# Performance work log

Hardware: AMD Instinct MI355X
Metric: run time of the kernel (lower is better)

The kernel has to match this reference:

```python
import jax, jax.numpy as jnp
import numpy as np

B, S, DIM, H, D = 2, 2048, 1024, 16, 64
WINDOW = 512
MAX_MEM_SEGMENTS = 1
ROPE_THETA = 10000.0


def _rope(t, pos):
    # lucidrains rotary-embedding-torch default: interleaved pairs
    d = t.shape[-1]
    inv_freq = 1.0 / (ROPE_THETA ** (jnp.arange(0, d, 2, dtype=jnp.float32) / d))
    freqs = pos[:, None].astype(jnp.float32) * inv_freq[None, :]        # [S, d/2]
    freqs = jnp.repeat(freqs, 2, axis=-1)                               # [S, d]
    cos, sin = jnp.cos(freqs), jnp.sin(freqs)
    t1, t2 = t[..., 0::2], t[..., 1::2]
    rot = jnp.stack((-t2, t1), axis=-1).reshape(t.shape)                # rotate_half
    return t * cos + rot * sin


def setup_inputs() -> dict:
    key = jax.random.key(0)
    ks = jax.random.split(key, 8)
    tokens = jax.random.normal(ks[0], (B, S, DIM), dtype=jnp.float32)
    value_residual = jax.random.normal(ks[1], (B, H, S, D), dtype=jnp.float32)
    episode_ids = jnp.sort(jax.random.randint(ks[2], (B, S), 0, 4), axis=-1)
    w = 0.02
    Wq = jax.random.normal(ks[3], (DIM, H * D), dtype=jnp.float32) * w
    Wkv = jax.random.normal(ks[4], (DIM, 2 * H * D), dtype=jnp.float32) * w
    Wo = jax.random.normal(ks[5], (H * D, DIM), dtype=jnp.float32) * w
    Wg = jax.random.normal(ks[6], (DIM, H), dtype=jnp.float32) * w
    Wmix = jax.random.normal(ks[7], (DIM, H), dtype=jnp.float32) * w
    return {"tokens": tokens, "value_residual": value_residual, "episode_ids": episode_ids,
            "Wq": Wq, "Wkv": Wkv, "Wo": Wo, "Wg": Wg, "Wmix": Wmix}


def reference(tokens, value_residual, episode_ids, Wq, Wkv, Wo, Wg, Wmix):
    b, s, _ = tokens.shape
    scale = D ** -0.5

    def split_heads(x):  # [b, n, h*d] -> [b, h, n, d]
        return x.reshape(b, s, H, D).transpose(0, 2, 1, 3)

    q = split_heads(tokens @ Wq)
    kv = tokens @ Wkv
    k, v = split_heads(kv[..., :H * D]), split_heads(kv[..., H * D:])

    q = q * scale

    # value-residual lerp: v.lerp(value_residual, mix)
    mix = jax.nn.sigmoid(jnp.einsum('bnd,dh->bhn', tokens, Wmix))[..., None]  # [b,h,n,1]
    v = v + mix * (value_residual - v)

    pos = jnp.arange(s)
    q = _rope(q, pos)
    k = _rope(k, pos)

    sim = jnp.einsum('bhid,bhjd->bhij', q, k)

    # fixed-window causal mask: masked where dist < 0 or dist > max_mem_segments*window
    dist = pos[:, None] - pos[None, :]
    win_mask = (dist < 0) | (dist > MAX_MEM_SEGMENTS * WINDOW)            # [s, s]
    ep_mask = episode_ids[:, :, None] != episode_ids[:, None, :]          # [b, s, s]
    mask = win_mask[None, None, :, :] | ep_mask[:, None, :, :]

    sim = jnp.where(mask, -jnp.finfo(sim.dtype).max, sim)
    attn = jax.nn.softmax(sim, axis=-1)
    out = jnp.einsum('bhij,bhjd->bhid', attn, v)

    # sigmoid value gating
    gate = jax.nn.sigmoid(jnp.einsum('bnd,dh->bhn', tokens, Wg))[..., None]
    out = out * gate

    out = out.transpose(0, 2, 1, 3).reshape(b, s, H * D)
    return out @ Wo
```

## Files before the change

kernel.cpp:

```cpp
#include <hip/hip_runtime.h>
#include <math.h>

#define BB 2
#define SS 2048
#define DIMM 1024
#define HH 16
#define DD 64
#define WINDOW 512

typedef __bf16 bf16x8 __attribute__((ext_vector_type(8)));
typedef __bf16 bf16x4 __attribute__((ext_vector_type(4)));
typedef float f32x4 __attribute__((ext_vector_type(4)));

__device__ __forceinline__ unsigned short f2bf(float f) {
    unsigned int u = __float_as_uint(f);
    u = (u + 0x7FFFu + ((u >> 16) & 1u)) >> 16;
    return (unsigned short)u;
}
__device__ __forceinline__ float bf2f(unsigned short u) {
    return __uint_as_float((unsigned int)u << 16);
}

__device__ __forceinline__ void async_cp16(unsigned short* lds_dst, const unsigned short* g_src) {
    __builtin_amdgcn_global_load_lds(
        (const __attribute__((address_space(1))) unsigned int*)g_src,
        (__attribute__((address_space(3))) unsigned int*)lds_dst, 16, 0, 0);
}

__global__ __launch_bounds__(256) void prep_all_kernel(
    const float* __restrict__ tokens, unsigned short* __restrict__ tokA,
    const float* __restrict__ Wq, const float* __restrict__ Wkv,
    const float* __restrict__ Wo, unsigned short* __restrict__ BtW,
    unsigned short* __restrict__ WotW,
    const float* __restrict__ Wg, const float* __restrict__ Wmix,
    unsigned short* __restrict__ wgmt,
    const int* __restrict__ ep, int* __restrict__ epstart,
    float2* __restrict__ ropetab)
{
    int bid = blockIdx.x;
    int tid = threadIdx.x;
    if (bid < 4096) {
        const float* src;
        unsigned short* dst;
        int C, bx, by;
        if (bid < 1024) {
            src = Wq; dst = BtW; C = 1024; bx = bid & 31; by = bid >> 5;
        } else if (bid < 3072) {
            int rel = bid - 1024;
            src = Wkv; dst = BtW + 1024 * 1024; C = 2048; bx = rel & 63; by = rel >> 6;
        } else {
            int rel = bid - 3072;
            src = Wo; dst = WotW; C = 1024; bx = rel & 31; by = rel >> 5;
        }
        const int R = 1024;
        __shared__ float t[32][33];
        int c0 = bx * 32, r0 = by * 32;
        int tx = tid & 31, ty = tid >> 5;
        #pragma unroll
        for (int u = 0; u < 4; ++u)
            t[ty + 8 * u][tx] = src[(size_t)(r0 + ty + 8 * u) * C + c0 + tx];
        __syncthreads();
        #pragma unroll
        for (int u = 0; u < 4; ++u)
            dst[(size_t)(c0 + ty + 8 * u) * R + r0 + tx] = f2bf(t[tx][ty + 8 * u]);
    } else if (bid < 6144) {
        const int n4 = (BB * SS * DIMM) / 4;
        for (int i = (bid - 4096) * 256 + tid; i < n4; i += 2048 * 256) {
            float4 v = ((const float4*)tokens)[i];
            ushort4 o;
            o.x = f2bf(v.x); o.y = f2bf(v.y); o.z = f2bf(v.z); o.w = f2bf(v.w);
            ((ushort4*)tokA)[i] = o;
        }
    } else if (bid < 6272) {
        int idx = (bid - 6144) * 256 + tid;
        int n = idx >> 10, k = idx & 1023;
        const float* src = (n < 16) ? Wg : Wmix;
        wgmt[idx] = f2bf(src[k * HH + (n & 15)]);
    } else if (bid < 6288) {
        int idx = (bid - 6272) * 256 + tid;
        int b = idx >> 11, i = idx & 2047;
        const int* e = ep + b * SS;
        int v = e[i];
        int lo = 0, hi = i;
        while (lo < hi) {
            int mid = (lo + hi) >> 1;
            if (e[mid] == v) hi = mid; else lo = mid + 1;
        }
        epstart[idx] = lo;
    } else {
        int idx = (bid - 6288) * 256 + tid;
        int s = idx >> 5, p = idx & 31;
        float invf = powf(10000.f, -(float)(2 * p) * (1.f / 64.f));
        float ang = (float)s * invf;
        float rr = ang - 6.2831853f * floorf(ang * 0.15915494f);
        float cs, sn;
        __sincosf(rr, &sn, &cs);
        ropetab[idx] = make_float2(cs, sn);
    }
}

__global__ __launch_bounds__(256) void projmix_kernel(
    const unsigned short* __restrict__ A, const unsigned short* __restrict__ Bt,
    unsigned short* __restrict__ qo, unsigned short* __restrict__ ko,
    unsigned short* __restrict__ vo,
    const unsigned short* __restrict__ wgmt,
    float* __restrict__ gate, float* __restrict__ mix)
{
    __shared__ unsigned short As[2][128 * 32];
    __shared__ unsigned short Bs[2][128 * 32];
    __shared__ float red[4][16][32];

    const int K = 1024;
    int bid = blockIdx.x;
    int tid = threadIdx.x;
    int lane = tid & 63;
    int wave = tid >> 6;
    int fr = lane & 15, hi = lane >> 4;

    if (bid < 768) {
        int nbase = (bid % 24) * 128;
        int mbase = (bid / 24) * 128;
        int wr = wave >> 1, wc = wave & 1;

        int srow = tid >> 2;
        int sp   = tid & 3;
        int scol = (sp ^ ((srow >> 1) & 3)) * 8;
        const unsigned short* agp0 = A  + (size_t)(mbase + srow) * K + scol;
        const unsigned short* agp1 = A  + (size_t)(mbase + srow + 64) * K + scol;
        const unsigned short* bgp0 = Bt + (size_t)(nbase + srow) * K + scol;
        const unsigned short* bgp1 = Bt + (size_t)(nbase + srow + 64) * K + scol;

        f32x4 acc[4][4];
        #pragma unroll
        for (int m_ = 0; m_ < 4; ++m_)
            #pragma unroll
            for (int n_ = 0; n_ < 4; ++n_)
                acc[m_][n_] = (f32x4){0.f, 0.f, 0.f, 0.f};

        int aidx[4], bidx[4];
        #pragma unroll
        for (int m_ = 0; m_ < 4; ++m_) {
            int row = wr * 64 + m_ * 16 + fr;
            aidx[m_] = row * 32 + (hi ^ ((row >> 1) & 3)) * 8;
        }
        #pragma unroll
        for (int n_ = 0; n_ < 4; ++n_) {
            int row = wc * 64 + n_ * 16 + fr;
            bidx[n_] = row * 32 + (hi ^ ((row >> 1) & 3)) * 8;
        }

        auto stage = [&](int buf, int k0) {
            async_cp16(&As[buf][tid * 8], agp0 + k0);
            async_cp16(&As[buf][2048 + tid * 8], agp1 + k0);
            async_cp16(&Bs[buf][tid * 8], bgp0 + k0);
            async_cp16(&Bs[buf][2048 + tid * 8], bgp1 + k0);
        };

        stage(0, 0);
        for (int k0 = 0; k0 < K; k0 += 32) {
            int cur = (k0 >> 5) & 1;
            __syncthreads();
            if (k0 + 32 < K) stage(cur ^ 1, k0 + 32);

            bf16x8 af[4], bfr[4];
            #pragma unroll
            for (int m_ = 0; m_ < 4; ++m_) af[m_] = *(const bf16x8*)&As[cur][aidx[m_]];
            #pragma unroll
            for (int n_ = 0; n_ < 4; ++n_) bfr[n_] = *(const bf16x8*)&Bs[cur][bidx[n_]];
            #pragma unroll
            for (int m_ = 0; m_ < 4; ++m_)
                #pragma unroll
                for (int n_ = 0; n_ < 4; ++n_)
                    acc[m_][n_] = __builtin_amdgcn_mfma_f32_16x16x32_bf16(
                        af[m_], bfr[n_], acc[m_][n_], 0, 0, 0);
        }

        #pragma unroll
        for (int m_ = 0; m_ < 4; ++m_) {
            #pragma unroll
            for (int n_ = 0; n_ < 4; ++n_) {
                int c = nbase + wc * 64 + n_ * 16 + fr;
                int cc = c & 1023, h = cc >> 6, d = cc & 63;
                unsigned short* dst = (c < 1024) ? qo : (c < 2048) ? ko : vo;
                #pragma unroll
                for (int j = 0; j < 4; ++j) {
                    int mg = mbase + wr * 64 + m_ * 16 + hi * 4 + j;
                    int b = mg >> 11, s = mg & 2047;
                    dst[(((size_t)b * HH + h) * SS + s) * DD + d] = f2bf(acc[m_][n_][j]);
                }
            }
        }
    } else {
        int mbase = (bid - 768) * 16;
        int kw = wave * 256;

        f32x4 acc[2];
        acc[0] = (f32x4){0.f, 0.f, 0.f, 0.f};
        acc[1] = (f32x4){0.f, 0.f, 0.f, 0.f};

        const unsigned short* a0 = A + (size_t)(mbase + fr) * 1024 + kw + hi * 8;
        const unsigned short* b0 = wgmt + (size_t)fr * 1024 + kw + hi * 8;
        const unsigned short* b1 = wgmt + (size_t)(16 + fr) * 1024 + kw + hi * 8;

        #pragma unroll 2
        for (int k = 0; k < 256; k += 32) {
            bf16x8 af0 = *(const bf16x8*)(a0 + k);
            bf16x8 bf0 = *(const bf16x8*)(b0 + k);
            bf16x8 bf1 = *(const bf16x8*)(b1 + k);
            acc[0] = __builtin_amdgcn_mfma_f32_16x16x32_bf16(af0, bf0, acc[0], 0, 0, 0);
            acc[1] = __builtin_amdgcn_mfma_f32_16x16x32_bf16(af0, bf1, acc[1], 0, 0, 0);
        }

        #pragma unroll
        for (int n_ = 0; n_ < 2; ++n_)
            #pragma unroll
            for (int j = 0; j < 4; ++j)
                red[wave][hi * 4 + j][n_ * 16 + fr] = acc[n_][j];
        __syncthreads();

        #pragma unroll
        for (int e = 0; e < 2; ++e) {
            int idx = tid * 2 + e;
            int r = idx >> 5, c = idx & 31;
            float s4 = red[0][r][c] + red[1][r][c] + red[2][r][c] + red[3][r][c];
            float sg = 1.f / (1.f + __expf(-s4));
            int mg = mbase + r;
            int b = mg >> 11, s = mg & 2047;
            int h = c & 15;
            float* dst = (c < 16) ? gate : mix;
            dst[((size_t)b * HH + h) * SS + s] = sg;
        }
    }
}

template<int BM, int BN>
__global__ __launch_bounds__(256) void gemm_mfma(
    const unsigned short* __restrict__ A, const unsigned short* __restrict__ Bt,
    float* __restrict__ C)
{
    const int K = 1024;
    constexpr int MFR = BM / 32;
    constexpr int NFR = BN / 32;
    int nbase = blockIdx.x * BN;
    int mbase = blockIdx.y * BM;

    int tid = threadIdx.x;
    int lane = tid & 63;
    int wave = tid >> 6;
    int wr = wave >> 1, wc = wave & 1;
    int fr = lane & 15, hi = lane >> 4;

    __shared__ unsigned short As[2][BM * 32];
    __shared__ unsigned short Bs[2][BN * 32];

    int srow = tid >> 2;
    int sp   = tid & 3;
    int scol = (sp ^ ((srow >> 1) & 3)) * 8;
    const unsigned short* agp0 = A  + (size_t)(mbase + srow) * K + scol;
    const unsigned short* agp1 = (BM == 128)
        ? A + (size_t)(mbase + srow + 64) * K + scol : agp0;
    const unsigned short* bgp0 = Bt + (size_t)(nbase + srow) * K + scol;
    const unsigned short* bgp1 = (BN == 128)
        ? Bt + (size_t)(nbase + srow + 64) * K + scol : bgp0;

    f32x4 acc[MFR][NFR];
    #pragma unroll
    for (int m_ = 0; m_ < MFR; ++m_)
        #pragma unroll
        for (int n_ = 0; n_ < NFR; ++n_)
            acc[m_][n_] = (f32x4){0.f, 0.f, 0.f, 0.f};

    int aidx[MFR], bidx[NFR];
    #pragma unroll
    for (int m_ = 0; m_ < MFR; ++m_) {
        int row = wr * (BM / 2) + m_ * 16 + fr;
        aidx[m_] = row * 32 + (hi ^ ((row >> 1) & 3)) * 8;
    }
    #pragma unroll
    for (int n_ = 0; n_ < NFR; ++n_) {
        int row = wc * (BN / 2) + n_ * 16 + fr;
        bidx[n_] = row * 32 + (hi ^ ((row >> 1) & 3)) * 8;
    }

    auto stage = [&](int buf, int k0) {
        async_cp16(&As[buf][tid * 8], agp0 + k0);
        if constexpr (BM == 128)
            async_cp16(&As[buf][2048 + tid * 8], agp1 + k0);
        async_cp16(&Bs[buf][tid * 8], bgp0 + k0);
        if constexpr (BN == 128)
            async_cp16(&Bs[buf][2048 + tid * 8], bgp1 + k0);
    };

    stage(0, 0);
    for (int k0 = 0; k0 < K; k0 += 32) {
        int cur = (k0 >> 5) & 1;
        __syncthreads();
        if (k0 + 32 < K) stage(cur ^ 1, k0 + 32);

        bf16x8 af[MFR], bfr[NFR];
        #pragma unroll
        for (int m_ = 0; m_ < MFR; ++m_) af[m_] = *(const bf16x8*)&As[cur][aidx[m_]];
        #pragma unroll
        for (int n_ = 0; n_ < NFR; ++n_) bfr[n_] = *(const bf16x8*)&Bs[cur][bidx[n_]];
        #pragma unroll
        for (int m_ = 0; m_ < MFR; ++m_)
            #pragma unroll
            for (int n_ = 0; n_ < NFR; ++n_)
                acc[m_][n_] = __builtin_amdgcn_mfma_f32_16x16x32_bf16(
                    af[m_], bfr[n_], acc[m_][n_], 0, 0, 0);
    }

    #pragma unroll
    for (int m_ = 0; m_ < MFR; ++m_) {
        #pragma unroll
        for (int n_ = 0; n_ < NFR; ++n_) {
            int c = nbase + wc * (BN / 2) + n_ * 16 + fr;
            #pragma unroll
            for (int j = 0; j < 4; ++j) {
                int mg = mbase + wr * (BM / 2) + m_ * 16 + hi * 4 + j;
                C[(size_t)mg * 1024 + c] = acc[m_][n_][j];
            }
        }
    }
}

__global__ __launch_bounds__(256) void rope_lerp_kernel(
    unsigned short* __restrict__ q, unsigned short* __restrict__ k,
    const unsigned short* __restrict__ v0, const float* __restrict__ vres,
    const float* __restrict__ mix, unsigned short* __restrict__ vt,
    const float2* __restrict__ ropetab)
{
    int st = blockIdx.x;
    int bh = blockIdx.y;
    int tid = threadIdx.x;
    int sl = tid >> 2;
    int dg = (tid & 3) * 16;
    int s = st * 64 + sl;
    size_t rowoff = ((size_t)bh * SS + s) * DD + dg;

    __shared__ unsigned short vtile[64][66];

    union { uint4 v[2]; unsigned short u[16]; } qa, ka, va;
    qa.v[0] = *(const uint4*)(q + rowoff);
    qa.v[1] = *(const uint4*)(q + rowoff + 8);
    ka.v[0] = *(const uint4*)(k + rowoff);
    ka.v[1] = *(const uint4*)(k + rowoff + 8);
    va.v[0] = *(const uint4*)(v0 + rowoff);
    va.v[1] = *(const uint4*)(v0 + rowoff + 8);
    float4 w[4];
    #pragma unroll
    for (int u = 0; u < 4; ++u) w[u] = *(const float4*)(vres + rowoff + 4 * u);
    float mx = mix[(size_t)bh * SS + s];
    const float2* tb = ropetab + (size_t)s * 32 + (dg >> 1);

    #pragma unroll
    for (int u = 0; u < 8; ++u) {
        float2 cssn = tb[u];
        float cs = cssn.x, sn = cssn.y;
        float x = bf2f(qa.u[2 * u]), y = bf2f(qa.u[2 * u + 1]);
        qa.u[2 * u]     = f2bf((x * cs - y * sn) * 0.125f);
        qa.u[2 * u + 1] = f2bf((y * cs + x * sn) * 0.125f);
        x = bf2f(ka.u[2 * u]); y = bf2f(ka.u[2 * u + 1]);
        ka.u[2 * u]     = f2bf(x * cs - y * sn);
        ka.u[2 * u + 1] = f2bf(y * cs + x * sn);
    }
    *(uint4*)(q + rowoff)     = qa.v[0];
    *(uint4*)(q + rowoff + 8) = qa.v[1];
    *(uint4*)(k + rowoff)     = ka.v[0];
    *(uint4*)(k + rowoff + 8) = ka.v[1];

    #pragma unroll
    for (int e = 0; e < 16; ++e) {
        float vv = bf2f(va.u[e]);
        float wr = ((const float*)w)[e];
        vtile[sl][dg + e] = f2bf(vv + mx * (wr - vv));
    }
    __syncthreads();

    int d = tid >> 2;
    int sseg = (tid & 3) * 16;
    union { uint4 v[2]; unsigned short u[16]; } ot;
    #pragma unroll
    for (int e = 0; e < 16; ++e) ot.u[e] = vtile[sseg + e][d];
    unsigned short* dst = vt + ((size_t)bh * DD + d) * SS + st * 64 + sseg;
    *(uint4*)dst = ot.v[0];
    *(uint4*)(dst + 8) = ot.v[1];
}

__global__ __launch_bounds__(512) void attn_mfma(
    const unsigned short* __restrict__ qbh, const unsigned short* __restrict__ kbh,
    const unsigned short* __restrict__ vt, const int* __restrict__ epstart,
    const float* __restrict__ gate, unsigned short* __restrict__ ao)
{
    int orig = blockIdx.x;
    int swz  = (orig & 7) * 64 + (orig >> 3);
    int bh = swz >> 4, qt = swz & 15;
    int b = bh >> 4, h = bh & 15;
    int q0 = qt * 128;
    int tid = threadIdx.x;
    int wave = tid >> 6, lane = tid & 63;
    int lq = lane & 15, lg = lane >> 4;
    int i = q0 + wave * 16 + lq;

    __shared__ unsigned short Ks[4096];
    __shared__ unsigned short Vs[4096];
    alignas(16) __shared__ unsigned short P_lds[8][16][72];

    int srow = tid >> 3;
    int sc = (((tid & 7) ^ (srow & 7)) << 3);
    const unsigned short* kS = kbh + ((size_t)bh * SS + srow) * DD + sc;
    const unsigned short* vS = vt + ((size_t)bh * DD + srow) * SS + sc;

    int fidx[4];
    #pragma unroll
    for (int n = 0; n < 4; ++n) {
        int r = 16 * n + lq;
        fidx[n] = r * 64 + ((lg ^ (r & 7)) << 3);
    }

    const unsigned short* qrow = qbh + ((size_t)bh * SS + i) * DD + lg * 8;
    bf16x8 bq0 = *(const bf16x8*)qrow;
    bf16x8 bq1 = *(const bf16x8*)(qrow + 32);

    int jmin = i - WINDOW;
    int es = epstart[b * SS + i];
    if (es > jmin) jmin = es;
    float gi = gate[(size_t)bh * SS + i];

    float m = -1e30f, l = 0.f;
    f32x4 o[4];
    #pragma unroll
    for (int n = 0; n < 4; ++n) o[n] = (f32x4){0.f, 0.f, 0.f, 0.f};

    int jt0 = (q0 >= 512) ? ((q0 - 512) >> 6) : 0;
    int jt1 = (q0 + 127) >> 6;
    int nt = jt1 - jt0 + 1;
    int jb0 = jt0 * 64;

    for (int u = 0; u < nt; ++u) {
        int jbase = jb0 + 64 * u;

        __syncthreads();
        async_cp16(&Ks[tid * 8], kS + (size_t)jbase * DD);
        async_cp16(&Vs[tid * 8], vS + jbase);
        __syncthreads();

        f32x4 acc[4];
        #pragma unroll
        for (int n = 0; n < 4; ++n) acc[n] = (f32x4){0.f, 0.f, 0.f, 0.f};
        __builtin_amdgcn_s_setprio(1);
        #pragma unroll
        for (int n = 0; n < 4; ++n) {
            bf16x8 kf0 = *(const bf16x8*)&Ks[fidx[n]];
            bf16x8 kf1 = *(const bf16x8*)&Ks[fidx[n] ^ 32];
            acc[n] = __builtin_amdgcn_mfma_f32_16x16x32_bf16(kf0, bq0, acc[n], 0, 0, 0);
            acc[n] = __builtin_amdgcn_mfma_f32_16x16x32_bf16(kf1, bq1, acc[n], 0, 0, 0);
        }
        __builtin_amdgcn_s_setprio(0);

        int jb = jbase + lg * 4;
        #pragma unroll
        for (int n = 0; n < 4; ++n)
            #pragma unroll
            for (int r = 0; r < 4; ++r) {
                int j = jb + 16 * n + r;
                if (j < jmin || j > i) acc[n][r] = -3e38f;
            }

        float tm = -3e38f;
        #pragma unroll
        for (int n = 0; n < 4; ++n)
            tm = fmaxf(tm, fmaxf(fmaxf(acc[n][0], acc[n][1]), fmaxf(acc[n][2], acc[n][3])));
        tm = fmaxf(tm, __shfl_xor(tm, 16, 64));
        tm = fmaxf(tm, __shfl_xor(tm, 32, 64));
        float mnew = fmaxf(m, tm);
        float scale = __expf(m - mnew);
        float ts = 0.f;
        #pragma unroll
        for (int n = 0; n < 4; ++n)
            #pragma unroll
            for (int r = 0; r < 4; ++r) {
                float p = __expf(acc[n][r] - mnew);
                acc[n][r] = p;
                ts += p;
            }
        ts += __shfl_xor(ts, 16, 64);
        ts += __shfl_xor(ts, 32, 64);
        l = l * scale + ts;
        m = mnew;
        #pragma unroll
        for (int n = 0; n < 4; ++n) o[n] = o[n] * scale;

        #pragma unroll
        for (int n = 0; n < 4; ++n) {
            bf16x4 pv;
            pv[0] = (__bf16)acc[n][0]; pv[1] = (__bf16)acc[n][1];
            pv[2] = (__bf16)acc[n][2]; pv[3] = (__bf16)acc[n][3];
            *(bf16x4*)&P_lds[wave][lq][16 * n + lg * 4] = pv;
        }
        bf16x8 bp0 = *(const bf16x8*)&P_lds[wave][lq][lg * 8];
        bf16x8 bp1 = *(const bf16x8*)&P_lds[wave][lq][32 + lg * 8];

        __builtin_amdgcn_s_setprio(1);
        #pragma unroll
        for (int n = 0; n < 4; ++n) {
            bf16x8 vf0 = *(const bf16x8*)&Vs[fidx[n]];
            bf16x8 vf1 = *(const bf16x8*)&Vs[fidx[n] ^ 32];
            o[n] = __builtin_amdgcn_mfma_f32_16x16x32_bf16(vf0, bp0, o[n], 0, 0, 0);
            o[n] = __builtin_amdgcn_mfma_f32_16x16x32_bf16(vf1, bp1, o[n], 0, 0, 0);
        }
        __builtin_amdgcn_s_setprio(0);
    }

    float g = gi / l;
    #pragma unroll
    for (int n = 0; n < 4; ++n) {
        bf16x4 ov;
        ov[0] = (__bf16)(o[n][0] * g); ov[1] = (__bf16)(o[n][1] * g);
        ov[2] = (__bf16)(o[n][2] * g); ov[3] = (__bf16)(o[n][3] * g);
        *(bf16x4*)(ao + (((size_t)b * SS + i) * HH + h) * DD + 16 * n + lg * 4) = ov;
    }
}

extern "C" void kernel_launch(void* const* d_in, const int* in_sizes, int n_in,
                              void* d_out, int out_size, void* d_ws, size_t ws_size,
                              hipStream_t stream)
{
    const float* tokens = (const float*)d_in[0];
    const float* vres   = (const float*)d_in[1];
    const int*   ep     = (const int*)d_in[2];
    const float* Wq     = (const float*)d_in[3];
    const float* Wkv    = (const float*)d_in[4];
    const float* Wo     = (const float*)d_in[5];
    const float* Wg     = (const float*)d_in[6];
    const float* Wmix   = (const float*)d_in[7];
    float* out = (float*)d_out;

    char* wsb = (char*)d_ws;
    unsigned short* qbh  = (unsigned short*)(wsb + 0);
    unsigned short* kbh  = (unsigned short*)(wsb + 8388608);
    unsigned short* vb0  = (unsigned short*)(wsb + 16777216);
    unsigned short* vtb  = (unsigned short*)(wsb + 25165824);
    unsigned short* aob  = (unsigned short*)(wsb + 33554432);
    unsigned short* tokA = (unsigned short*)(wsb + 41943040);
    unsigned short* BtW  = (unsigned short*)(wsb + 50331648);
    float* gatep = (float*)(wsb + 56623104);
    float* mixp  = (float*)(wsb + 56885248);
    int*   epst  = (int*)(wsb + 57147392);
    unsigned short* wgmt = (unsigned short*)(wsb + 57163776);
    unsigned short* WotW = (unsigned short*)(wsb + 57229312);
    float2* ropetab = (float2*)(wsb + 59326464);

    prep_all_kernel<<<6544, 256, 0, stream>>>(tokens, tokA, Wq, Wkv, Wo, BtW, WotW,
                                              Wg, Wmix, wgmt, ep, epst, ropetab);
    projmix_kernel<<<1024, 256, 0, stream>>>(tokA, BtW, qbh, kbh, vb0,
                                             wgmt, gatep, mixp);
    rope_lerp_kernel<<<dim3(SS / 64, BB * HH), 256, 0, stream>>>(qbh, kbh, vb0, vres, mixp, vtb, ropetab);
    attn_mfma<<<512, 512, 0, stream>>>(qbh, kbh, vtb, epst, gatep, aob);

    gemm_mfma<128, 64><<<dim3(16, 32), 256, 0, stream>>>(aob, WotW, out);
}
```

Baseline: 110.8 us.

## Fuse Q rotary embedding into attention kernel and alias projmix shared memory

```diff
diff --git a/kernel.cpp b/kernel.cpp
--- a/kernel.cpp
+++ b/kernel.cpp
@@ -106,9 +106,10 @@
     const unsigned short* __restrict__ wgmt,
     float* __restrict__ gate, float* __restrict__ mix)
 {
-    __shared__ unsigned short As[2][128 * 32];
-    __shared__ unsigned short Bs[2][128 * 32];
-    __shared__ float red[4][16][32];
+    __shared__ char smem[32768];
+    unsigned short* As = (unsigned short*)smem;
+    unsigned short* Bs = (unsigned short*)(smem + 16384);
+    float (*red)[16][32] = (float (*)[16][32])smem;
 
     const int K = 1024;
     int bid = blockIdx.x;
@@ -150,10 +151,10 @@
         }
 
         auto stage = [&](int buf, int k0) {
-            async_cp16(&As[buf][tid * 8], agp0 + k0);
-            async_cp16(&As[buf][2048 + tid * 8], agp1 + k0);
-            async_cp16(&Bs[buf][tid * 8], bgp0 + k0);
-            async_cp16(&Bs[buf][2048 + tid * 8], bgp1 + k0);
+            async_cp16(&As[buf * 4096 + tid * 8], agp0 + k0);
+            async_cp16(&As[buf * 4096 + 2048 + tid * 8], agp1 + k0);
+            async_cp16(&Bs[buf * 4096 + tid * 8], bgp0 + k0);
+            async_cp16(&Bs[buf * 4096 + 2048 + tid * 8], bgp1 + k0);
         };
 
         stage(0, 0);
@@ -164,9 +165,9 @@
 
             bf16x8 af[4], bfr[4];
             #pragma unroll
-            for (int m_ = 0; m_ < 4; ++m_) af[m_] = *(const bf16x8*)&As[cur][aidx[m_]];
-            #pragma unroll
-            for (int n_ = 0; n_ < 4; ++n_) bfr[n_] = *(const bf16x8*)&Bs[cur][bidx[n_]];
+            for (int m_ = 0; m_ < 4; ++m_) af[m_] = *(const bf16x8*)&As[cur * 4096 + aidx[m_]];
+            #pragma unroll
+            for (int n_ = 0; n_ < 4; ++n_) bfr[n_] = *(const bf16x8*)&Bs[cur * 4096 + bidx[n_]];
             #pragma unroll
             for (int m_ = 0; m_ < 4; ++m_)
                 #pragma unroll
@@ -325,7 +326,7 @@
 }
 
 __global__ __launch_bounds__(256) void rope_lerp_kernel(
-    unsigned short* __restrict__ q, unsigned short* __restrict__ k,
+    unsigned short* __restrict__ k,
     const unsigned short* __restrict__ v0, const float* __restrict__ vres,
     const float* __restrict__ mix, unsigned short* __restrict__ vt,
     const float2* __restrict__ ropetab)
@@ -340,9 +341,7 @@
 
     __shared__ unsigned short vtile[64][66];
 
-    union { uint4 v[2]; unsigned short u[16]; } qa, ka, va;
-    qa.v[0] = *(const uint4*)(q + rowoff);
-    qa.v[1] = *(const uint4*)(q + rowoff + 8);
+    union { uint4 v[2]; unsigned short u[16]; } ka, va;
     ka.v[0] = *(const uint4*)(k + rowoff);
     ka.v[1] = *(const uint4*)(k + rowoff + 8);
     va.v[0] = *(const uint4*)(v0 + rowoff);
@@ -357,15 +356,10 @@
     for (int u = 0; u < 8; ++u) {
         float2 cssn = tb[u];
         float cs = cssn.x, sn = cssn.y;
-        float x = bf2f(qa.u[2 * u]), y = bf2f(qa.u[2 * u + 1]);
-        qa.u[2 * u]     = f2bf((x * cs - y * sn) * 0.125f);
-        qa.u[2 * u + 1] = f2bf((y * cs + x * sn) * 0.125f);
-        x = bf2f(ka.u[2 * u]); y = bf2f(ka.u[2 * u + 1]);
+        float x = bf2f(ka.u[2 * u]), y = bf2f(ka.u[2 * u + 1]);
         ka.u[2 * u]     = f2bf(x * cs - y * sn);
         ka.u[2 * u + 1] = f2bf(y * cs + x * sn);
     }
-    *(uint4*)(q + rowoff)     = qa.v[0];
-    *(uint4*)(q + rowoff + 8) = qa.v[1];
     *(uint4*)(k + rowoff)     = ka.v[0];
     *(uint4*)(k + rowoff + 8) = ka.v[1];
 
@@ -390,7 +384,8 @@
 __global__ __launch_bounds__(512) void attn_mfma(
     const unsigned short* __restrict__ qbh, const unsigned short* __restrict__ kbh,
     const unsigned short* __restrict__ vt, const int* __restrict__ epstart,
-    const float* __restrict__ gate, unsigned short* __restrict__ ao)
+    const float* __restrict__ gate, unsigned short* __restrict__ ao,
+    const float2* __restrict__ ropetab)
 {
     int orig = blockIdx.x;
     int swz  = (orig & 7) * 64 + (orig >> 3);
@@ -419,8 +414,25 @@
     }
 
     const unsigned short* qrow = qbh + ((size_t)bh * SS + i) * DD + lg * 8;
-    bf16x8 bq0 = *(const bf16x8*)qrow;
-    bf16x8 bq1 = *(const bf16x8*)(qrow + 32);
+    union { bf16x8 v; __bf16 e[8]; } uq0, uq1;
+    uq0.v = *(const bf16x8*)qrow;
+    uq1.v = *(const bf16x8*)(qrow + 32);
+    {
+        const float2* tbq = ropetab + (size_t)i * 32 + lg * 4;
+        #pragma unroll
+        for (int p = 0; p < 4; ++p) {
+            float2 t0 = tbq[p];
+            float x = (float)uq0.e[2 * p], y = (float)uq0.e[2 * p + 1];
+            uq0.e[2 * p]     = (__bf16)((x * t0.x - y * t0.y) * 0.125f);
+            uq0.e[2 * p + 1] = (__bf16)((y * t0.x + x * t0.y) * 0.125f);
+            float2 t1 = tbq[16 + p];
+            x = (float)uq1.e[2 * p]; y = (float)uq1.e[2 * p + 1];
+            uq1.e[2 * p]     = (__bf16)((x * t1.x - y * t1.y) * 0.125f);
+            uq1.e[2 * p + 1] = (__bf16)((y * t1.x + x * t1.y) * 0.125f);
+        }
+    }
+    bf16x8 bq0 = uq0.v;
+    bf16x8 bq1 = uq1.v;
 
     int jmin = i - WINDOW;
     int es = epstart[b * SS + i];
@@ -555,8 +567,8 @@
                                               Wg, Wmix, wgmt, ep, epst, ropetab);
     projmix_kernel<<<1024, 256, 0, stream>>>(tokA, BtW, qbh, kbh, vb0,
                                              wgmt, gatep, mixp);
-    rope_lerp_kernel<<<dim3(SS / 64, BB * HH), 256, 0, stream>>>(qbh, kbh, vb0, vres, mixp, vtb, ropetab);
-    attn_mfma<<<512, 512, 0, stream>>>(qbh, kbh, vtb, epst, gatep, aob);
+    rope_lerp_kernel<<<dim3(SS / 64, BB * HH), 256, 0, stream>>>(kbh, vb0, vres, mixp, vtb, ropetab);
+    attn_mfma<<<512, 512, 0, stream>>>(qbh, kbh, vtb, epst, gatep, aob, ropetab);
 
     gemm_mfma<128, 64><<<dim3(16, 32), 256, 0, stream>>>(aob, WotW, out);
 }
```

Measured after the change: 110.7 us. No clear change (-0.1%).
